# Performance work log

Hardware: AMD Instinct MI355X
Metric: run time of the kernel (lower is better)

The kernel has to match this reference:

```python
import jax, jax.numpy as jnp
import numpy as np

N_USERS, N_ITEMS = 100000, 50000
K = 5 * 20          # multi_factor * top_k
D = 64              # embedding_dim
B = 8192
CAT = 2 * K * D     # 12800
HID = CAT // 100    # 128


def setup_inputs() -> dict:
    key = jax.random.key(0)
    ks = jax.random.split(key, 12)
    return {
        "user_idxs": jax.random.randint(ks[0], (B,), 0, N_USERS),
        "item_idxs": jax.random.randint(ks[1], (B,), 0, N_ITEMS),
        "user_idx_tensor": jax.random.randint(ks[2], (N_USERS, K), 0, N_USERS),
        "item_idx_tensor": jax.random.randint(ks[3], (N_ITEMS, K), 0, N_ITEMS),
        "user_scr_tensor": jax.random.uniform(ks[4], (N_USERS, K), dtype=jnp.float32),
        "item_scr_tensor": jax.random.uniform(ks[5], (N_ITEMS, K), dtype=jnp.float32),
        "user_emb": jax.random.normal(ks[6], (N_USERS, D), dtype=jnp.float32) * 0.1,
        "item_emb": jax.random.normal(ks[7], (N_ITEMS, D), dtype=jnp.float32) * 0.1,
        "W1": jax.random.normal(ks[8], (CAT, HID), dtype=jnp.float32) * 0.02,
        "b1": jnp.zeros((HID,), dtype=jnp.float32),
        "W2": jax.random.normal(ks[9], (HID, 1), dtype=jnp.float32) * 0.02,
        "b2": jnp.zeros((1,), dtype=jnp.float32),
    }


def _side(idxs, idx_tensor, scr_tensor, emb_table):
    neighs = idx_tensor[idxs]                 # [B, K] neighbor ids
    neigh_emb = emb_table[neighs]             # [B, K, D]
    neigh_scr = scr_tensor[neighs]            # [B, K, K]
    scored = jnp.einsum('bkj,bjd->bkd', neigh_scr, neigh_emb)  # [B, K, D]
    return scored.reshape(scored.shape[0], -1)                 # [B, K*D]


def reference(user_idxs, item_idxs, user_idx_tensor, item_idx_tensor,
              user_scr_tensor, item_scr_tensor, user_emb, item_emb,
              W1, b1, W2, b2):
    u = _side(user_idxs, user_idx_tensor, user_scr_tensor, user_emb)
    v = _side(item_idxs, item_idx_tensor, item_scr_tensor, item_emb)
    x = jnp.concatenate([u, v], axis=-1)      # [B, 2*K*D]
    h = jax.nn.relu(x @ W1 + b1)
    o = jax.nn.relu(h @ W2 + b2)
    return jax.nn.sigmoid(o).squeeze(-1)      # [B]
```

## Files before the change

### kernel.cpp

```cpp
#include <hip/hip_runtime.h>
#include <hip/hip_bf16.h>
#include <math.h>

constexpr int KN  = 100;
constexpr int DE  = 64;
constexpr int CAT = 2 * KN * DE;
constexpr int HID = 128;

typedef __bf16          bf16x8   __attribute__((ext_vector_type(8)));
typedef float           f32x4    __attribute__((ext_vector_type(4)));
typedef unsigned short  ushort8v __attribute__((ext_vector_type(8)));
typedef unsigned short  ushort4v __attribute__((ext_vector_type(4)));

static __device__ __forceinline__ unsigned short f2bf(float f) {
    __hip_bfloat16 h = __float2bfloat16(f);
    return *reinterpret_cast<unsigned short*>(&h);
}

static __device__ __forceinline__ bf16x8 mk_frag(ushort4v lo, ushort4v hi) {
    union { ushort8v u; bf16x8 b; } c;
    c.u = (ushort8v){ lo[0], lo[1], lo[2], lo[3], hi[0], hi[1], hi[2], hi[3] };
    return c.b;
}

__global__ __launch_bounds__(256) void cvt4(
    const float* __restrict__ a0, unsigned short* __restrict__ o0, int n0,
    const float* __restrict__ a1, unsigned short* __restrict__ o1, int n1,
    const float* __restrict__ a2, unsigned short* __restrict__ o2, int n2,
    const float* __restrict__ a3, unsigned short* __restrict__ o3, int n3)
{
    const float* in; unsigned short* out; int n4;
    switch (blockIdx.y) {
        case 0:  in = a0; out = o0; n4 = n0; break;
        case 1:  in = a1; out = o1; n4 = n1; break;
        case 2:  in = a2; out = o2; n4 = n2; break;
        default: in = a3; out = o3; n4 = n3; break;
    }
    for (int i = blockIdx.x * 256 + threadIdx.x; i < n4; i += gridDim.x * 256) {
        float4 v = ((const float4*)in)[i];
        ushort4v o = { f2bf(v.x), f2bf(v.y), f2bf(v.z), f2bf(v.w) };
        ((ushort4v*)out)[i] = o;
    }
}

__global__ __launch_bounds__(256) void prep_w1t(
    const float* __restrict__ W1, unsigned short* __restrict__ w1t)
{
    __shared__ unsigned short T[HID][72];
    const int t  = threadIdx.x;
    const int k0 = blockIdx.x * 64;

    for (int idx = t; idx < 64 * HID; idx += 256) {
        int kk = idx >> 7, n = idx & 127;
        T[n][kk] = f2bf(W1[(size_t)(k0 + kk) * HID + n]);
    }
    __syncthreads();
    for (int idx = t; idx < HID * 16; idx += 256) {
        int n = idx >> 4, c4 = idx & 15;
        *(ushort4v*)&w1t[(size_t)n * CAT + k0 + c4 * 4] =
            *(const ushort4v*)&T[n][c4 * 4];
    }
}

__global__ __launch_bounds__(256) void einsum_mfma(
    const int* __restrict__ u_idx, const int* __restrict__ i_idx,
    const int* __restrict__ u_nbt, const int* __restrict__ i_nbt,
    const unsigned short* __restrict__ u_scr, const unsigned short* __restrict__ i_scr,
    const unsigned short* __restrict__ u_emb, const unsigned short* __restrict__ i_emb,
    unsigned short* __restrict__ xb, int b0)
{
    __shared__ __align__(16) unsigned short ET[64][136];
    __shared__ int nb[KN];

    const int t    = threadIdx.x;
    const int side = blockIdx.y;
    const int b    = b0 + blockIdx.x;

    const int*            idxs = side ? i_idx : u_idx;
    const int*            nbt  = side ? i_nbt : u_nbt;
    const unsigned short* scr  = side ? i_scr : u_scr;
    const unsigned short* emb  = side ? i_emb : u_emb;

    const ushort4v z4 = {0, 0, 0, 0};

    const int center = idxs[b];
    if (t < KN) nb[t] = nbt[(size_t)center * KN + t];

    for (int idx = t; idx < 64 * 7; idx += 256) {
        int r = idx / 7, c = idx - r * 7;
        *(ushort4v*)&ET[r][100 + c * 4] = z4;
    }
    __syncthreads();

    for (int idx = t; idx < 25 * 16; idx += 256) {
        int d4 = idx / 25, j0 = idx - d4 * 25;
        ushort4v v0 = *(const ushort4v*)(emb + (size_t)nb[j0 * 4 + 0] * DE + d4 * 4);
        ushort4v v1 = *(const ushort4v*)(emb + (size_t)nb[j0 * 4 + 1] * DE + d4 * 4);
        ushort4v v2 = *(const ushort4v*)(emb + (size_t)nb[j0 * 4 + 2] * DE + d4 * 4);
        ushort4v v3 = *(const ushort4v*)(emb + (size_t)nb[j0 * 4 + 3] * DE + d4 * 4);
        ushort4v o0 = { v0[0], v1[0], v2[0], v3[0] };
        ushort4v o1 = { v0[1], v1[1], v2[1], v3[1] };
        ushort4v o2 = { v0[2], v1[2], v2[2], v3[2] };
        ushort4v o3 = { v0[3], v1[3], v2[3], v3[3] };
        *(ushort4v*)&ET[d4 * 4 + 0][j0 * 4] = o0;
        *(ushort4v*)&ET[d4 * 4 + 1][j0 * 4] = o1;
        *(ushort4v*)&ET[d4 * 4 + 2][j0 * 4] = o2;
        *(ushort4v*)&ET[d4 * 4 + 3][j0 * 4] = o3;
    }
    __syncthreads();

    const int w  = t >> 6;
    const int l  = t & 63;
    const int cl = l & 15;
    const int rg = l >> 4;

    const unsigned short* srow[7];
    #pragma unroll
    for (int mt = 0; mt < 7; ++mt) {
        int kr = mt * 16 + cl;
        if (kr > KN - 1) kr = KN - 1;
        srow[mt] = scr + (size_t)nb[kr] * KN;
    }

    f32x4 acc[7];
    #pragma unroll
    for (int m = 0; m < 7; ++m) acc[m] = (f32x4){0.f, 0.f, 0.f, 0.f};

    #pragma unroll
    for (int ks = 0; ks < 4; ++ks) {
        const int k0 = ks * 32 + rg * 8;
        bf16x8 bfrag = *(const bf16x8*)&ET[w * 16 + cl][k0];
        #pragma unroll
        for (int mt = 0; mt < 7; ++mt) {
            ushort4v lo, hi;
            if (ks < 3) {
                lo = *(const ushort4v*)(srow[mt] + k0);
                hi = *(const ushort4v*)(srow[mt] + k0 + 4);
            } else if (rg == 0) {
                lo = *(const ushort4v*)(srow[mt] + 96);
                hi = z4;
            } else {
                lo = z4; hi = z4;
            }
            bf16x8 afrag = mk_frag(lo, hi);
            acc[mt] = __builtin_amdgcn_mfma_f32_16x16x32_bf16(afrag, bfrag, acc[mt], 0, 0, 0);
        }
    }
    __syncthreads();

    unsigned short* X = &ET[0][0];
    #pragma unroll
    for (int mt = 0; mt < 7; ++mt) {
        #pragma unroll
        for (int rr = 0; rr < 4; ++rr) {
            int k = mt * 16 + rg * 4 + rr;
            if (k < KN) X[k * 72 + w * 16 + cl] = f2bf(acc[mt][rr]);
        }
    }
    __syncthreads();

    unsigned short* xr = xb + (size_t)blockIdx.x * CAT + side * (KN * DE);
    for (int idx = t; idx < KN * 8; idx += 256) {
        int r = idx >> 3, c8 = idx & 7;
        __builtin_nontemporal_store(*(const ushort8v*)&X[r * 72 + c8 * 8],
                                    (ushort8v*)&xr[r * DE + c8 * 8]);
    }
}

__global__ __launch_bounds__(256) void mlp_kernel(
    const unsigned short* __restrict__ xb, const unsigned short* __restrict__ w1t,
    const float* __restrict__ b1, const float* __restrict__ W2,
    const float* __restrict__ b2, float* __restrict__ out, int b0)
{
    __shared__ unsigned short A[32][136];
    __shared__ unsigned short Bt[HID][136];
    __shared__ float red[4][32];

    const int t    = threadIdx.x;
    const int w    = t >> 6;
    const int l    = t & 63;
    const int cl   = l & 15;
    const int rgrp = l >> 4;
    const int row0 = blockIdx.x * 32;

    f32x4 acc[2][2];
    #pragma unroll
    for (int i = 0; i < 2; ++i)
        #pragma unroll
        for (int j = 0; j < 2; ++j)
            acc[i][j] = (f32x4){0.f, 0.f, 0.f, 0.f};

    for (int kb = 0; kb < CAT; kb += 128) {
        if (kb) __syncthreads();
        #pragma unroll
        for (int i = 0; i < 2; ++i) {
            int c = t + i * 256;
            int r = c >> 4, c16 = c & 15;
            *(ushort8v*)&A[r][c16 * 8] = __builtin_nontemporal_load(
                (const ushort8v*)&xb[(size_t)(row0 + r) * CAT + kb + c16 * 8]);
        }
        #pragma unroll
        for (int i = 0; i < 8; ++i) {
            int c = t + i * 256;
            int n = c >> 4, c16 = c & 15;
            *(ushort8v*)&Bt[n][c16 * 8] =
                *(const ushort8v*)&w1t[(size_t)n * CAT + kb + c16 * 8];
        }
        __syncthreads();

        #pragma unroll
        for (int ks = 0; ks < 4; ++ks) {
            const int kcol = ks * 32 + rgrp * 8;
            bf16x8 a0 = *(const bf16x8*)&A[cl][kcol];
            bf16x8 a1 = *(const bf16x8*)&A[16 + cl][kcol];
            bf16x8 v0 = *(const bf16x8*)&Bt[w * 32 + cl][kcol];
            bf16x8 v1 = *(const bf16x8*)&Bt[w * 32 + 16 + cl][kcol];
            acc[0][0] = __builtin_amdgcn_mfma_f32_16x16x32_bf16(a0, v0, acc[0][0], 0, 0, 0);
            acc[0][1] = __builtin_amdgcn_mfma_f32_16x16x32_bf16(a0, v1, acc[0][1], 0, 0, 0);
            acc[1][0] = __builtin_amdgcn_mfma_f32_16x16x32_bf16(a1, v0, acc[1][0], 0, 0, 0);
            acc[1][1] = __builtin_amdgcn_mfma_f32_16x16x32_bf16(a1, v1, acc[1][1], 0, 0, 0);
        }
    }

    const float b1c0 = b1[w * 32 + cl];
    const float b1c1 = b1[w * 32 + 16 + cl];
    const float w2c0 = W2[w * 32 + cl];
    const float w2c1 = W2[w * 32 + 16 + cl];

    #pragma unroll
    for (int mt = 0; mt < 2; ++mt) {
        #pragma unroll
        for (int r = 0; r < 4; ++r) {
            float h0 = fmaxf(acc[mt][0][r] + b1c0, 0.f);
            float h1 = fmaxf(acc[mt][1][r] + b1c1, 0.f);
            float p  = fmaf(h0, w2c0, h1 * w2c1);
            p += __shfl_xor(p, 1, 64);
            p += __shfl_xor(p, 2, 64);
            p += __shfl_xor(p, 4, 64);
            p += __shfl_xor(p, 8, 64);
            if (cl == 0) red[w][mt * 16 + rgrp * 4 + r] = p;
        }
    }
    __syncthreads();
    if (t < 32) {
        float o = red[0][t] + red[1][t] + red[2][t] + red[3][t] + b2[0];
        o = fmaxf(o, 0.f);
        out[b0 + row0 + t] = 1.f / (1.f + expf(-o));
    }
}

extern "C" void kernel_launch(void* const* d_in, const int* in_sizes, int n_in,
                              void* d_out, int out_size, void* d_ws, size_t ws_size,
                              hipStream_t stream)
{
    const int*   user_idxs = (const int*)d_in[0];
    const int*   item_idxs = (const int*)d_in[1];
    const int*   user_nbt  = (const int*)d_in[2];
    const int*   item_nbt  = (const int*)d_in[3];
    const float* user_scr  = (const float*)d_in[4];
    const float* item_scr  = (const float*)d_in[5];
    const float* user_emb  = (const float*)d_in[6];
    const float* item_emb  = (const float*)d_in[7];
    const float* W1        = (const float*)d_in[8];
    const float* b1        = (const float*)d_in[9];
    const float* W2        = (const float*)d_in[10];
    const float* b2        = (const float*)d_in[11];
    float*       out       = (float*)d_out;

    const int B = in_sizes[0];

    char* p = (char*)d_ws;
    unsigned short* w1t   = (unsigned short*)p;  p += (size_t)HID * CAT * 2;
    unsigned short* us_bf = (unsigned short*)p;  p += (size_t)in_sizes[4] * 2;
    unsigned short* is_bf = (unsigned short*)p;  p += (size_t)in_sizes[5] * 2;
    unsigned short* ue_bf = (unsigned short*)p;  p += (size_t)in_sizes[6] * 2;
    unsigned short* ie_bf = (unsigned short*)p;  p += (size_t)in_sizes[7] * 2;
    unsigned short* xb    = (unsigned short*)p;
    const size_t fixed = (size_t)(p - (char*)d_ws);

    const size_t row_bytes = (size_t)CAT * sizeof(unsigned short);
    long max_rows = (long)((ws_size - fixed) / row_bytes);
    int chunk = (int)((max_rows / 32) * 32);
    if (chunk > B) chunk = B;
    if (chunk < 32) chunk = 32;

    prep_w1t<<<CAT / 64, 256, 0, stream>>>(W1, w1t);
    cvt4<<<dim3(512, 4), 256, 0, stream>>>(
        user_scr, us_bf, in_sizes[4] / 4,
        item_scr, is_bf, in_sizes[5] / 4,
        user_emb, ue_bf, in_sizes[6] / 4,
        item_emb, ie_bf, in_sizes[7] / 4);

    for (int b0 = 0; b0 < B; b0 += chunk) {
        int rows = (B - b0 < chunk) ? (B - b0) : chunk;
        einsum_mfma<<<dim3(rows, 2), 256, 0, stream>>>(
            user_idxs, item_idxs, user_nbt, item_nbt,
            us_bf, is_bf, ue_bf, ie_bf, xb, b0);
        mlp_kernel<<<rows / 32, 256, 0, stream>>>(
            xb, w1t, b1, W2, b2, out, b0);
    }
}
```

Measured before the change: 344.9 us.

## Chunk batch to keep intermediate in cache and halve MLP row tile

Caps the batch chunk at 4096 rows so the bf16 intermediate activations (about 100 MB per chunk) have a better chance of staying in the last-level cache between the einsum and MLP kernels. Nontemporal stores and loads on that buffer are replaced with regular ones to match. The MLP kernel now handles 16 rows per block instead of 32, doubling the block count for more parallelism. In exchange, each W1 tile is reloaded twice as often relative to the MFMA work done, and extra kernel launches are added per chunk.

```diff
diff --git a/kernel.cpp b/kernel.cpp
--- a/kernel.cpp
+++ b/kernel.cpp
@@ -6,6 +6,7 @@
 constexpr int DE  = 64;
 constexpr int CAT = 2 * KN * DE;
 constexpr int HID = 128;
+constexpr int CHUNK = 4096;
 
 typedef __bf16          bf16x8   __attribute__((ext_vector_type(8)));
 typedef float           f32x4    __attribute__((ext_vector_type(4)));
@@ -162,8 +163,7 @@
     unsigned short* xr = xb + (size_t)blockIdx.x * CAT + side * (KN * DE);
     for (int idx = t; idx < KN * 8; idx += 256) {
         int r = idx >> 3, c8 = idx & 7;
-        __builtin_nontemporal_store(*(const ushort8v*)&X[r * 72 + c8 * 8],
-                                    (ushort8v*)&xr[r * DE + c8 * 8]);
+        *(ushort8v*)&xr[r * DE + c8 * 8] = *(const ushort8v*)&X[r * 72 + c8 * 8];
     }
 }
 
@@ -172,32 +172,27 @@
     const float* __restrict__ b1, const float* __restrict__ W2,
     const float* __restrict__ b2, float* __restrict__ out, int b0)
 {
-    __shared__ unsigned short A[32][136];
+    __shared__ unsigned short A[16][136];
     __shared__ unsigned short Bt[HID][136];
-    __shared__ float red[4][32];
+    __shared__ float red[4][16];
 
     const int t    = threadIdx.x;
     const int w    = t >> 6;
     const int l    = t & 63;
     const int cl   = l & 15;
     const int rgrp = l >> 4;
-    const int row0 = blockIdx.x * 32;
-
-    f32x4 acc[2][2];
-    #pragma unroll
-    for (int i = 0; i < 2; ++i)
-        #pragma unroll
-        for (int j = 0; j < 2; ++j)
-            acc[i][j] = (f32x4){0.f, 0.f, 0.f, 0.f};
+    const int row0 = blockIdx.x * 16;
+
+    f32x4 acc[2];
+    acc[0] = (f32x4){0.f, 0.f, 0.f, 0.f};
+    acc[1] = (f32x4){0.f, 0.f, 0.f, 0.f};
 
     for (int kb = 0; kb < CAT; kb += 128) {
         if (kb) __syncthreads();
-        #pragma unroll
-        for (int i = 0; i < 2; ++i) {
-            int c = t + i * 256;
-            int r = c >> 4, c16 = c & 15;
-            *(ushort8v*)&A[r][c16 * 8] = __builtin_nontemporal_load(
-                (const ushort8v*)&xb[(size_t)(row0 + r) * CAT + kb + c16 * 8]);
+        {
+            int r = t >> 4, c16 = t & 15;
+            *(ushort8v*)&A[r][c16 * 8] =
+                *(const ushort8v*)&xb[(size_t)(row0 + r) * CAT + kb + c16 * 8];
         }
         #pragma unroll
         for (int i = 0; i < 8; ++i) {
@@ -212,13 +207,10 @@
         for (int ks = 0; ks < 4; ++ks) {
             const int kcol = ks * 32 + rgrp * 8;
             bf16x8 a0 = *(const bf16x8*)&A[cl][kcol];
-            bf16x8 a1 = *(const bf16x8*)&A[16 + cl][kcol];
             bf16x8 v0 = *(const bf16x8*)&Bt[w * 32 + cl][kcol];
             bf16x8 v1 = *(const bf16x8*)&Bt[w * 32 + 16 + cl][kcol];
-            acc[0][0] = __builtin_amdgcn_mfma_f32_16x16x32_bf16(a0, v0, acc[0][0], 0, 0, 0);
-            acc[0][1] = __builtin_amdgcn_mfma_f32_16x16x32_bf16(a0, v1, acc[0][1], 0, 0, 0);
-            acc[1][0] = __builtin_amdgcn_mfma_f32_16x16x32_bf16(a1, v0, acc[1][0], 0, 0, 0);
-            acc[1][1] = __builtin_amdgcn_mfma_f32_16x16x32_bf16(a1, v1, acc[1][1], 0, 0, 0);
+            acc[0] = __builtin_amdgcn_mfma_f32_16x16x32_bf16(a0, v0, acc[0], 0, 0, 0);
+            acc[1] = __builtin_amdgcn_mfma_f32_16x16x32_bf16(a0, v1, acc[1], 0, 0, 0);
         }
     }
 
@@ -228,21 +220,18 @@
     const float w2c1 = W2[w * 32 + 16 + cl];
 
     #pragma unroll
-    for (int mt = 0; mt < 2; ++mt) {
-        #pragma unroll
-        for (int r = 0; r < 4; ++r) {
-            float h0 = fmaxf(acc[mt][0][r] + b1c0, 0.f);
-            float h1 = fmaxf(acc[mt][1][r] + b1c1, 0.f);
-            float p  = fmaf(h0, w2c0, h1 * w2c1);
-            p += __shfl_xor(p, 1, 64);
-            p += __shfl_xor(p, 2, 64);
-            p += __shfl_xor(p, 4, 64);
-            p += __shfl_xor(p, 8, 64);
-            if (cl == 0) red[w][mt * 16 + rgrp * 4 + r] = p;
-        }
-    }
-    __syncthreads();
-    if (t < 32) {
+    for (int r = 0; r < 4; ++r) {
+        float h0 = fmaxf(acc[0][r] + b1c0, 0.f);
+        float h1 = fmaxf(acc[1][r] + b1c1, 0.f);
+        float p  = fmaf(h0, w2c0, h1 * w2c1);
+        p += __shfl_xor(p, 1, 64);
+        p += __shfl_xor(p, 2, 64);
+        p += __shfl_xor(p, 4, 64);
+        p += __shfl_xor(p, 8, 64);
+        if (cl == 0) red[w][rgrp * 4 + r] = p;
+    }
+    __syncthreads();
+    if (t < 16) {
         float o = red[0][t] + red[1][t] + red[2][t] + red[3][t] + b2[0];
         o = fmaxf(o, 0.f);
         out[b0 + row0 + t] = 1.f / (1.f + expf(-o));
@@ -281,6 +270,7 @@
     const size_t row_bytes = (size_t)CAT * sizeof(unsigned short);
     long max_rows = (long)((ws_size - fixed) / row_bytes);
     int chunk = (int)((max_rows / 32) * 32);
+    if (chunk > CHUNK) chunk = CHUNK;
     if (chunk > B) chunk = B;
     if (chunk < 32) chunk = 32;
 
@@ -296,7 +286,7 @@
         einsum_mfma<<<dim3(rows, 2), 256, 0, stream>>>(
             user_idxs, item_idxs, user_nbt, item_nbt,
             us_bf, is_bf, ue_bf, ie_bf, xb, b0);
-        mlp_kernel<<<rows / 32, 256, 0, stream>>>(
+        mlp_kernel<<<(rows + 15) / 16, 256, 0, stream>>>(
             xb, w1t, b1, W2, b2, out, b0);
     }
 }
```

After: 423.2 us. +22.7%, slower.

## Double-buffer MLP LDS tiles and launch one MLP kernel over all rows

Applied to the files above, without the earlier changes.

Double-buffers the A and W1 tiles in shared memory so the next K-slice is loaded while MFMAs run on the current one, with one barrier per step. The einsum still runs in fixed 4096-row chunks, but each chunk now writes at its own offset in the intermediate buffer, and a single MLP launch then covers the whole batch. Nontemporal loads and stores on the intermediate are replaced with ordinary ones. The shared-memory footprint roughly doubles, which can lower occupancy. The workspace size is no longer checked and must now hold the full batch of intermediate rows.

```diff
diff --git a/kernel.cpp b/kernel.cpp
--- a/kernel.cpp
+++ b/kernel.cpp
@@ -6,6 +6,7 @@
 constexpr int DE  = 64;
 constexpr int CAT = 2 * KN * DE;
 constexpr int HID = 128;
+constexpr int CHUNK = 4096;
 
 typedef __bf16          bf16x8   __attribute__((ext_vector_type(8)));
 typedef float           f32x4    __attribute__((ext_vector_type(4)));
@@ -162,18 +163,17 @@
     unsigned short* xr = xb + (size_t)blockIdx.x * CAT + side * (KN * DE);
     for (int idx = t; idx < KN * 8; idx += 256) {
         int r = idx >> 3, c8 = idx & 7;
-        __builtin_nontemporal_store(*(const ushort8v*)&X[r * 72 + c8 * 8],
-                                    (ushort8v*)&xr[r * DE + c8 * 8]);
-    }
-}
-
-__global__ __launch_bounds__(256) void mlp_kernel(
+        *(ushort8v*)&xr[r * DE + c8 * 8] = *(const ushort8v*)&X[r * 72 + c8 * 8];
+    }
+}
+
+__global__ __launch_bounds__(256) void mlp_fused(
     const unsigned short* __restrict__ xb, const unsigned short* __restrict__ w1t,
     const float* __restrict__ b1, const float* __restrict__ W2,
-    const float* __restrict__ b2, float* __restrict__ out, int b0)
-{
-    __shared__ unsigned short A[32][136];
-    __shared__ unsigned short Bt[HID][136];
+    const float* __restrict__ b2, float* __restrict__ out)
+{
+    __shared__ unsigned short A[2][32][136];
+    __shared__ unsigned short Bt[2][HID][136];
     __shared__ float red[4][32];
 
     const int t    = threadIdx.x;
@@ -183,43 +183,50 @@
     const int rgrp = l >> 4;
     const int row0 = blockIdx.x * 32;
 
-    f32x4 acc[2][2];
-    #pragma unroll
-    for (int i = 0; i < 2; ++i)
-        #pragma unroll
-        for (int j = 0; j < 2; ++j)
-            acc[i][j] = (f32x4){0.f, 0.f, 0.f, 0.f};
-
-    for (int kb = 0; kb < CAT; kb += 128) {
-        if (kb) __syncthreads();
+    auto stage = [&](int buf, int kb) {
         #pragma unroll
         for (int i = 0; i < 2; ++i) {
             int c = t + i * 256;
             int r = c >> 4, c16 = c & 15;
-            *(ushort8v*)&A[r][c16 * 8] = __builtin_nontemporal_load(
-                (const ushort8v*)&xb[(size_t)(row0 + r) * CAT + kb + c16 * 8]);
+            *(ushort8v*)&A[buf][r][c16 * 8] =
+                *(const ushort8v*)&xb[(size_t)(row0 + r) * CAT + kb + c16 * 8];
         }
         #pragma unroll
         for (int i = 0; i < 8; ++i) {
             int c = t + i * 256;
             int n = c >> 4, c16 = c & 15;
-            *(ushort8v*)&Bt[n][c16 * 8] =
+            *(ushort8v*)&Bt[buf][n][c16 * 8] =
                 *(const ushort8v*)&w1t[(size_t)n * CAT + kb + c16 * 8];
         }
-        __syncthreads();
-
+    };
+
+    f32x4 acc[2][2];
+    #pragma unroll
+    for (int i = 0; i < 2; ++i)
+        #pragma unroll
+        for (int j = 0; j < 2; ++j)
+            acc[i][j] = (f32x4){0.f, 0.f, 0.f, 0.f};
+
+    stage(0, 0);
+    __syncthreads();
+
+    constexpr int NS = CAT / 128;
+    for (int s = 0; s < NS; ++s) {
+        const int cur = s & 1;
+        if (s + 1 < NS) stage(cur ^ 1, (s + 1) * 128);
         #pragma unroll
         for (int ks = 0; ks < 4; ++ks) {
             const int kcol = ks * 32 + rgrp * 8;
-            bf16x8 a0 = *(const bf16x8*)&A[cl][kcol];
-            bf16x8 a1 = *(const bf16x8*)&A[16 + cl][kcol];
-            bf16x8 v0 = *(const bf16x8*)&Bt[w * 32 + cl][kcol];
-            bf16x8 v1 = *(const bf16x8*)&Bt[w * 32 + 16 + cl][kcol];
+            bf16x8 a0 = *(const bf16x8*)&A[cur][cl][kcol];
+            bf16x8 a1 = *(const bf16x8*)&A[cur][16 + cl][kcol];
+            bf16x8 v0 = *(const bf16x8*)&Bt[cur][w * 32 + cl][kcol];
+            bf16x8 v1 = *(const bf16x8*)&Bt[cur][w * 32 + 16 + cl][kcol];
             acc[0][0] = __builtin_amdgcn_mfma_f32_16x16x32_bf16(a0, v0, acc[0][0], 0, 0, 0);
             acc[0][1] = __builtin_amdgcn_mfma_f32_16x16x32_bf16(a0, v1, acc[0][1], 0, 0, 0);
             acc[1][0] = __builtin_amdgcn_mfma_f32_16x16x32_bf16(a1, v0, acc[1][0], 0, 0, 0);
             acc[1][1] = __builtin_amdgcn_mfma_f32_16x16x32_bf16(a1, v1, acc[1][1], 0, 0, 0);
         }
+        __syncthreads();
     }
 
     const float b1c0 = b1[w * 32 + cl];
@@ -245,7 +252,7 @@
     if (t < 32) {
         float o = red[0][t] + red[1][t] + red[2][t] + red[3][t] + b2[0];
         o = fmaxf(o, 0.f);
-        out[b0 + row0 + t] = 1.f / (1.f + expf(-o));
+        out[row0 + t] = 1.f / (1.f + expf(-o));
     }
 }
 
@@ -276,13 +283,6 @@
     unsigned short* ue_bf = (unsigned short*)p;  p += (size_t)in_sizes[6] * 2;
     unsigned short* ie_bf = (unsigned short*)p;  p += (size_t)in_sizes[7] * 2;
     unsigned short* xb    = (unsigned short*)p;
-    const size_t fixed = (size_t)(p - (char*)d_ws);
-
-    const size_t row_bytes = (size_t)CAT * sizeof(unsigned short);
-    long max_rows = (long)((ws_size - fixed) / row_bytes);
-    int chunk = (int)((max_rows / 32) * 32);
-    if (chunk > B) chunk = B;
-    if (chunk < 32) chunk = 32;
 
     prep_w1t<<<CAT / 64, 256, 0, stream>>>(W1, w1t);
     cvt4<<<dim3(512, 4), 256, 0, stream>>>(
@@ -291,12 +291,11 @@
         user_emb, ue_bf, in_sizes[6] / 4,
         item_emb, ie_bf, in_sizes[7] / 4);
 
-    for (int b0 = 0; b0 < B; b0 += chunk) {
-        int rows = (B - b0 < chunk) ? (B - b0) : chunk;
+    for (int b0 = 0; b0 < B; b0 += CHUNK) {
+        int rows = (B - b0 < CHUNK) ? (B - b0) : CHUNK;
         einsum_mfma<<<dim3(rows, 2), 256, 0, stream>>>(
             user_idxs, item_idxs, user_nbt, item_nbt,
-            us_bf, is_bf, ue_bf, ie_bf, xb, b0);
-        mlp_kernel<<<rows / 32, 256, 0, stream>>>(
-            xb, w1t, b1, W2, b2, out, b0);
-    }
-}
+            us_bf, is_bf, ue_bf, ie_bf, xb + (size_t)b0 * CAT, b0);
+    }
+    mlp_fused<<<B / 32, 256, 0, stream>>>(xb, w1t, b1, W2, b2, out);
+}
```

Measured after the change: 378.0 us. +9.6%, slower.
